# Kernel optimization log

Measured on AMD Instinct MI355X. Metric: run time of the kernel, lower is better.

Reference implementation:

```python
import jax, jax.numpy as jnp
import numpy as np

GROUP_SIZE = 8
REQUIRED_ZEROS = 4


def _dorefa_quantize(x, bits):
    # tanh-normalize-round
    t = jnp.tanh(x).astype(jnp.float32)
    y = t / jnp.max(jnp.abs(t))
    delta = float(2 ** (bits - 1) - 1)
    _y = jnp.round(y * delta)

    out_c, in_c, h, w = _y.shape
    if in_c < GROUP_SIZE:
        return _y / delta

    g = in_c // GROUP_SIZE
    keep = GROUP_SIZE - REQUIRED_ZEROS  # keep at most 4 non-zeros per group

    # [out_c, g*8, h, w] -> [out_c, g, h, w, 8] (group axis last for top_k)
    yg = _y[:, : g * GROUP_SIZE].reshape(out_c, g, GROUP_SIZE, h, w)
    yg = jnp.transpose(yg, (0, 1, 3, 4, 2))

    # The torch loop zeroes the smallest-|v| non-zeros until >=4 zeros per
    # group. Equivalently: keep only the `keep` largest-|v| entries of each
    # group (zeros have |v|=0, so groups already having >=4 zeros are
    # unchanged). Fully vectorized via batched top-k + one-hot mask.
    absv = jnp.abs(yg)
    _, idx = jax.lax.top_k(absv, keep)                      # [o,g,h,w,keep]
    mask = jax.nn.one_hot(idx, GROUP_SIZE, dtype=yg.dtype).sum(axis=-2)
    yg = yg * mask                                          # [o,g,h,w,8]

    yg = jnp.transpose(yg, (0, 1, 4, 2, 3)).reshape(out_c, g * GROUP_SIZE, h, w)
    out = jnp.concatenate([yg, _y[:, g * GROUP_SIZE :]], axis=1) if g * GROUP_SIZE < in_c else yg
    return out / delta


def setup_inputs() -> dict:
    key = jax.random.key(0)
    x = jax.random.normal(key, (2048, 2048, 3, 3), dtype=jnp.float32)
    return {"x": x, "bits": 8}


def reference(x, bits):
    return _dorefa_quantize(x, bits)
```

## Files before the change

### kernel.cpp

```cpp
#include <hip/hip_runtime.h>
#include <math.h>

#define HW        9
#define GROUP     8
#define KEEP      4
#define DELTA     127.0f
#define INV_DELTA (1.0f / 127.0f)
#define GB_FLOATS 72

__global__ void maxabs_kernel(const float4* __restrict__ x, unsigned* __restrict__ ws, int n4) {
    __shared__ float red[4];
    float m = 0.0f;
    int stride = gridDim.x * blockDim.x;
    #pragma unroll 4
    for (int i = blockIdx.x * blockDim.x + threadIdx.x; i < n4; i += stride) {
        float4 v = x[i];
        m = fmaxf(m, fmaxf(fmaxf(fabsf(v.x), fabsf(v.y)),
                           fmaxf(fabsf(v.z), fabsf(v.w))));
    }
    #pragma unroll
    for (int off = 32; off > 0; off >>= 1)
        m = fmaxf(m, __shfl_down(m, off, 64));
    int wave = threadIdx.x >> 6;
    if ((threadIdx.x & 63) == 0) red[wave] = m;
    __syncthreads();
    if (threadIdx.x == 0) {
        float b = fmaxf(fmaxf(red[0], red[1]), fmaxf(red[2], red[3]));
        atomicMax(ws, __float_as_uint(b));
    }
}

__device__ __attribute__((noinline)) float ref_rz(float xx, float M) {
    float td = (float)tanh((double)xx);
    float y  = td / M;
    return rintf(y * DELTA);
}

__device__ __forceinline__ float fast_tanh(float x) {
    float ax  = fabsf(x);
    float axc = fminf(ax, 10.0f);
    float E   = __expf(2.0f * axc);
    float num = E - 1.0f;
    float den = E + 1.0f;
    float r0  = __builtin_amdgcn_rcpf(den);
    float r   = r0 * fmaf(-den, r0, 2.0f);
    float tl  = copysignf(num * r, x);
    float s = x * x;
    float p = fmaf(s, 0.0035921280f, -0.0088632358f);
    p = fmaf(s, p, 0.021869488f);
    p = fmaf(s, p, -0.053968254f);
    p = fmaf(s, p, 0.13333334f);
    p = fmaf(s, p, -0.33333334f);
    float ts = fmaf(x * s, p, x);
    return (ax <= 0.5f) ? ts : tl;
}

__global__ void quant_kernel(const float4* __restrict__ x,
                             float4* __restrict__ out,
                             const unsigned* __restrict__ ws,
                             int n_gb) {
    __shared__ float sM, sC;
    if (threadIdx.x == 0) {
        float mm = (float)tanh((double)__uint_as_float(*ws));
        sM = mm;
        sC = (float)(127.0 / (double)mm);
    }
    __syncthreads();
    float M = sM, C = sC;

    int gb = blockIdx.x * blockDim.x + threadIdx.x;
    if (gb >= n_gb) return;

    const float4* p = x   + (size_t)gb * (GB_FLOATS / 4);
    float4*       q = out + (size_t)gb * (GB_FLOATS / 4);

    float f[GB_FLOATS];
    #pragma unroll
    for (int k = 0; k < GB_FLOATS / 4; ++k) {
        float4 v = p[k];
        f[4 * k + 0] = v.x; f[4 * k + 1] = v.y;
        f[4 * k + 2] = v.z; f[4 * k + 3] = v.w;
    }

    #pragma unroll
    for (int hw = 0; hw < HW; ++hw) {
        float v8[GROUP], a8[GROUP];
        #pragma unroll
        for (int j = 0; j < GROUP; ++j) {
            float xx = f[j * HW + hw];
            float t  = fast_tanh(xx);
            float z  = t * C;
            float rz = rintf(z);
            float d  = 0.5f - fabsf(z - rz);
            if (d < fmaf(2e-6f, fabsf(z), 5e-7f))
                rz = ref_rz(xx, M);
            v8[j] = rz;
            a8[j] = fabsf(rz);
        }
        int rank[GROUP] = {0, 0, 0, 0, 0, 0, 0, 0};
        #pragma unroll
        for (int i = 0; i < GROUP; ++i) {
            #pragma unroll
            for (int j = i + 1; j < GROUP; ++j) {
                bool ge = (a8[i] >= a8[j]);
                rank[j] += ge ? 1 : 0;
                rank[i] += ge ? 0 : 1;
            }
        }
        #pragma unroll
        for (int j = 0; j < GROUP; ++j) {
            f[j * HW + hw] = (rank[j] < KEEP) ? (v8[j] * INV_DELTA) : 0.0f;
        }
    }

    #pragma unroll
    for (int k = 0; k < GB_FLOATS / 4; ++k) {
        float4 v;
        v.x = f[4 * k + 0]; v.y = f[4 * k + 1];
        v.z = f[4 * k + 2]; v.w = f[4 * k + 3];
        q[k] = v;
    }
}

extern "C" void kernel_launch(void* const* d_in, const int* in_sizes, int n_in,
                              void* d_out, int out_size, void* d_ws, size_t ws_size,
                              hipStream_t stream) {
    const float* x = (const float*)d_in[0];
    float* out = (float*)d_out;
    unsigned* ws = (unsigned*)d_ws;

    int n = in_sizes[0];
    int n4 = n / 4;
    int n_gb = n / GB_FLOATS;

    hipMemsetAsync(ws, 0, sizeof(unsigned), stream);

    maxabs_kernel<<<2048, 256, 0, stream>>>((const float4*)x, ws, n4);

    int blocks = (n_gb + 255) / 256;
    quant_kernel<<<blocks, 256, 0, stream>>>((const float4*)x, (float4*)out, ws, n_gb);
}
```

Before: 307.4 us.

## Stage quant tiles through LDS with direct global-to-LDS loads and coalesced stores

Replaces the per-thread 72-float register load/store (strided, uncoalesced across lanes) with per-wave tiles of 32 group-blocks loaded directly into LDS via global_load_lds, then computes each (group,hw) cell per lane from LDS and writes back with coalesced nontemporal vector stores. The aim is fully coalesced global access and lower register pressure, which allows more occupancy. In exchange it uses about 36KB of LDS per block, which can cap occupancy. It also adds LDS bank conflicts from the stride-9 access and requires each wave's full tile to be in bounds.

New measurement: 295.0 us. 4.0% less time.

```diff
diff --git a/kernel.cpp b/kernel.cpp
--- a/kernel.cpp
+++ b/kernel.cpp
@@ -7,6 +7,14 @@
 #define DELTA     127.0f
 #define INV_DELTA (1.0f / 127.0f)
 #define GB_FLOATS 72
+
+#define GB_TILE   32
+#define TILE_F    (GB_TILE * GB_FLOATS)
+#define TILE_CH   (TILE_F / 256)
+#define CELLS     (GB_TILE * HW)
+#define WPB       4
+
+typedef float f32x4 __attribute__((ext_vector_type(4)));
 
 __global__ void maxabs_kernel(const float4* __restrict__ x, unsigned* __restrict__ ws, int n4) {
     __shared__ float red[4];
@@ -55,10 +63,11 @@
     return (ax <= 0.5f) ? ts : tl;
 }
 
-__global__ void quant_kernel(const float4* __restrict__ x,
-                             float4* __restrict__ out,
+__global__ __launch_bounds__(256, 4) void quant_kernel(const float* __restrict__ x,
+                             float* __restrict__ out,
                              const unsigned* __restrict__ ws,
                              int n_gb) {
+    __shared__ float lds[WPB][TILE_F];
     __shared__ float sM, sC;
     if (threadIdx.x == 0) {
         float mm = (float)tanh((double)__uint_as_float(*ws));
@@ -68,57 +77,67 @@
     __syncthreads();
     float M = sM, C = sC;
 
-    int gb = blockIdx.x * blockDim.x + threadIdx.x;
-    if (gb >= n_gb) return;
+    const int wv   = threadIdx.x >> 6;
+    const int lane = threadIdx.x & 63;
+    const int tile = blockIdx.x * WPB + wv;
+    if (tile * GB_TILE >= n_gb) return;
 
-    const float4* p = x   + (size_t)gb * (GB_FLOATS / 4);
-    float4*       q = out + (size_t)gb * (GB_FLOATS / 4);
-
-    float f[GB_FLOATS];
-    #pragma unroll
-    for (int k = 0; k < GB_FLOATS / 4; ++k) {
-        float4 v = p[k];
-        f[4 * k + 0] = v.x; f[4 * k + 1] = v.y;
-        f[4 * k + 2] = v.z; f[4 * k + 3] = v.w;
-    }
+    const size_t base = (size_t)tile * TILE_F;
+    const float* src  = x + base;
+    float* ldsw       = &lds[wv][0];
 
     #pragma unroll
-    for (int hw = 0; hw < HW; ++hw) {
-        float v8[GROUP], a8[GROUP];
-        #pragma unroll
-        for (int j = 0; j < GROUP; ++j) {
-            float xx = f[j * HW + hw];
-            float t  = fast_tanh(xx);
-            float z  = t * C;
-            float rz = rintf(z);
-            float d  = 0.5f - fabsf(z - rz);
-            if (d < fmaf(2e-6f, fabsf(z), 5e-7f))
-                rz = ref_rz(xx, M);
-            v8[j] = rz;
-            a8[j] = fabsf(rz);
-        }
-        int rank[GROUP] = {0, 0, 0, 0, 0, 0, 0, 0};
-        #pragma unroll
-        for (int i = 0; i < GROUP; ++i) {
+    for (int k = 0; k < TILE_CH; ++k) {
+        __builtin_amdgcn_global_load_lds(
+            (__attribute__((address_space(1))) void*)(src + k * 256 + lane * 4),
+            (__attribute__((address_space(3))) void*)(ldsw + k * 256),
+            16, 0, 0);
+    }
+    asm volatile("s_waitcnt vmcnt(0)" ::: "memory");
+    __builtin_amdgcn_sched_barrier(0);
+
+    for (int c = 0; c < (CELLS + 63) / 64; ++c) {
+        int ci = lane + 64 * c;
+        if (ci < CELLS) {
+            int gb = ci / 9;
+            int hw = ci - gb * 9;
+            float* cell = ldsw + gb * GB_FLOATS + hw;
+
+            float v8[GROUP], a8[GROUP];
             #pragma unroll
-            for (int j = i + 1; j < GROUP; ++j) {
-                bool ge = (a8[i] >= a8[j]);
-                rank[j] += ge ? 1 : 0;
-                rank[i] += ge ? 0 : 1;
+            for (int j = 0; j < GROUP; ++j) {
+                float xx = cell[9 * j];
+                float t  = fast_tanh(xx);
+                float z  = t * C;
+                float rz = rintf(z);
+                float d  = 0.5f - fabsf(z - rz);
+                if (d < fmaf(2e-6f, fabsf(z), 5e-7f))
+                    rz = ref_rz(xx, M);
+                v8[j] = rz;
+                a8[j] = fabsf(rz);
             }
-        }
-        #pragma unroll
-        for (int j = 0; j < GROUP; ++j) {
-            f[j * HW + hw] = (rank[j] < KEEP) ? (v8[j] * INV_DELTA) : 0.0f;
+            int rank[GROUP] = {0, 0, 0, 0, 0, 0, 0, 0};
+            #pragma unroll
+            for (int i = 0; i < GROUP; ++i) {
+                #pragma unroll
+                for (int j = i + 1; j < GROUP; ++j) {
+                    bool ge = (a8[i] >= a8[j]);
+                    rank[j] += ge ? 1 : 0;
+                    rank[i] += ge ? 0 : 1;
+                }
+            }
+            #pragma unroll
+            for (int j = 0; j < GROUP; ++j)
+                cell[9 * j] = (rank[j] < KEEP) ? (v8[j] * INV_DELTA) : 0.0f;
         }
     }
+    __builtin_amdgcn_sched_barrier(0);
 
+    f32x4* dst4       = (f32x4*)(out + base);
+    const f32x4* l4   = (const f32x4*)ldsw;
     #pragma unroll
-    for (int k = 0; k < GB_FLOATS / 4; ++k) {
-        float4 v;
-        v.x = f[4 * k + 0]; v.y = f[4 * k + 1];
-        v.z = f[4 * k + 2]; v.w = f[4 * k + 3];
-        q[k] = v;
+    for (int k = 0; k < TILE_CH; ++k) {
+        __builtin_nontemporal_store(l4[k * 64 + lane], &dst4[k * 64 + lane]);
     }
 }
 
@@ -137,6 +156,6 @@
 
     maxabs_kernel<<<2048, 256, 0, stream>>>((const float4*)x, ws, n4);
 
-    int blocks = (n_gb + 255) / 256;
-    quant_kernel<<<blocks, 256, 0, stream>>>((const float4*)x, (float4*)out, ws, n_gb);
+    int blocks_q = (n_gb + GB_TILE * WPB - 1) / (GB_TILE * WPB);
+    quant_kernel<<<blocks_q, 256, 0, stream>>>(x, out, ws, n_gb);
 }
```
